# Kernel tuning notes

Measured on AMD Instinct MI355X. Metric: run time of the kernel, lower is better.

## Reference

```python
import jax, jax.numpy as jnp
import numpy as np

HIDDEN = 2048
HEADS = 16
HEAD_DIM = HIDDEN // HEADS  # 128
B, S = 2, 2048
SCALE = 1.0 / np.sqrt(HEAD_DIM)


def setup_inputs() -> dict:
    key = jax.random.key(0)
    ks = jax.random.split(key, 9)
    x = jax.random.normal(ks[0], (B, S, HIDDEN), dtype=jnp.float32)
    # causal mask, broadcastable to [B, 1(group), H, S, S]
    mask = jnp.tril(jnp.ones((S, S), dtype=bool))[None, None, None, :, :]
    mask = jnp.broadcast_to(mask, (B, 1, 1, S, S))
    s = 0.02
    Wq = jax.random.normal(ks[1], (HIDDEN, HIDDEN), dtype=jnp.float32) * s
    bq = jnp.zeros((HIDDEN,), dtype=jnp.float32)
    Wk = jax.random.normal(ks[2], (HIDDEN, HEAD_DIM), dtype=jnp.float32) * s
    bk = jnp.zeros((HEAD_DIM,), dtype=jnp.float32)
    Wv = jax.random.normal(ks[3], (HIDDEN, HEAD_DIM), dtype=jnp.float32) * s
    bv = jnp.zeros((HEAD_DIM,), dtype=jnp.float32)
    Wo = jax.random.normal(ks[4], (HIDDEN, HIDDEN), dtype=jnp.float32) * s
    bo = jnp.zeros((HIDDEN,), dtype=jnp.float32)
    return {"x": x, "mask": mask, "Wq": Wq, "bq": bq, "Wk": Wk, "bk": bk,
            "Wv": Wv, "bv": bv, "Wo": Wo, "bo": bo}


def reference(x, mask, Wq, bq, Wk, bk, Wv, bv, Wo, bo):
    b, s, _ = x.shape
    q = (x @ Wq + bq).reshape(b, s, HEADS, HEAD_DIM)   # [b,s,h,d]
    k = x @ Wk + bk                                    # [b,t,d] single shared KV head
    v = x @ Wv + bv                                    # [b,t,d]
    # scores: [b, h, s, t]; add group dim to match mask [b,1,h,s,t]
    scores = jnp.einsum('bshd,btd->bhst', q, k) * SCALE
    scores = scores[:, None]                            # [b,1,h,s,t]
    scores = jnp.where(mask, scores, jnp.float32(-jnp.inf))
    att = jax.nn.softmax(scores, axis=-1)[:, 0]         # [b,h,s,t] (dropout eval = identity)
    out = jnp.einsum('bhst,btd->bshd', att, v).reshape(b, s, HIDDEN)
    return out @ Wo + bo
```

## Files before the change

kernel.cpp:

```cpp
#include <hip/hip_runtime.h>


#define HIDDEN 2048
#define NHEADS 16
#define HDIM 128
#define BATCH 2
#define SEQ 2048
#define SCALE_L2E 0.1275258653864023f

typedef __attribute__((ext_vector_type(8))) short bfrag;
typedef __attribute__((ext_vector_type(4))) float facc;

__device__ __forceinline__ unsigned short f2bf(float f) {
  unsigned int u = __float_as_uint(f);
  u += 0x7fffu + ((u >> 16) & 1u);
  return (unsigned short)(u >> 16);
}

__device__ __forceinline__ unsigned int cvt_pk_bf16(float lo, float hi) {
  unsigned int r;
  asm("v_cvt_pk_bf16_f32 %0, %1, %2" : "=v"(r) : "v"(lo), "v"(hi));
  return r;
}

__device__ __forceinline__ void gl_lds16(const void* g, void* l) {
  __builtin_amdgcn_global_load_lds(
      (const __attribute__((address_space(1))) void*)g,
      (__attribute__((address_space(3))) void*)l, 16, 0, 0);
}

__global__ __launch_bounds__(256) void cvt_bf16(const float* __restrict__ in,
                                                unsigned int* __restrict__ out, int n4) {
  int i = blockIdx.x * 256 + threadIdx.x;
  if (i >= n4) return;
  float4 v = ((const float4*)in)[i];
  uint2 o = {cvt_pk_bf16(v.x, v.y), cvt_pk_bf16(v.z, v.w)};
  ((uint2*)out)[i] = o;
}

__global__ __launch_bounds__(256) void transpose_cvt2(const float* __restrict__ W0,
                                                      short* __restrict__ T0,
                                                      const float* __restrict__ W1,
                                                      short* __restrict__ T1,
                                                      int K, int N) {
  const float* W = blockIdx.z ? W1 : W0;
  short* WT = blockIdx.z ? T1 : T0;
  __shared__ float t[32][33];
  int tx = threadIdx.x & 31, ty = threadIdx.x >> 5;
  int n0 = blockIdx.x * 32, k0 = blockIdx.y * 32;
#pragma unroll
  for (int j = 0; j < 4; ++j)
    t[ty + j * 8][tx] = W[(size_t)(k0 + ty + j * 8) * N + n0 + tx];
  __syncthreads();
#pragma unroll
  for (int j = 0; j < 4; ++j)
    WT[(size_t)(n0 + ty + j * 8) * K + k0 + tx] = (short)f2bf(t[tx][ty + j * 8]);
}

#define GEMM_STAGE(buf, kt, A, BT, Kdim)                                       \
  _Pragma("unroll") for (int it = 0; it < 4; ++it) {                           \
    int bc = (w * 4 + it) * 64;                                                \
    int C = bc + l;                                                            \
    int row = C >> 3, c = C & 7;                                               \
    int gofs = (kt) * 64 + ((c ^ (row & 7)) << 3);                             \
    gl_lds16((A) + (size_t)(m0 + row) * (Kdim) + gofs, &Al[buf][bc * 8]);      \
    gl_lds16((BT) + (size_t)(n0 + row) * (Kdim) + gofs, &Bl[buf][bc * 8]);     \
  }

#define GEMM_PIPE_LOOP(A, BT, Kdim)                                            \
  facc acc[4][4] = {};                                                         \
  const int nkt = (Kdim) >> 6;                                                 \
  GEMM_STAGE(0, 0, A, BT, Kdim)                                                \
  __syncthreads();                                                             \
  for (int kt = 0; kt < nkt; ++kt) {                                           \
    const int cur = kt & 1;                                                    \
    if (kt + 1 < nkt) { GEMM_STAGE(cur ^ 1, kt + 1, A, BT, Kdim) }             \
    __builtin_amdgcn_s_setprio(1);                                             \
    _Pragma("unroll") for (int ks = 0; ks < 2; ++ks) {                         \
      bfrag af[4], bf[4];                                                      \
      _Pragma("unroll") for (int mt = 0; mt < 4; ++mt) {                       \
        int row = wr * 64 + mt * 16 + l15;                                     \
        int c = ks * 4 + l4;                                                   \
        af[mt] = *(const bfrag*)&Al[cur][row * 64 + ((c ^ (row & 7)) << 3)];   \
      }                                                                        \
      _Pragma("unroll") for (int nt = 0; nt < 4; ++nt) {                       \
        int row = wc * 64 + nt * 16 + l15;                                     \
        int c = ks * 4 + l4;                                                   \
        bf[nt] = *(const bfrag*)&Bl[cur][row * 64 + ((c ^ (row & 7)) << 3)];   \
      }                                                                        \
      _Pragma("unroll") for (int mt = 0; mt < 4; ++mt)                         \
          _Pragma("unroll") for (int nt = 0; nt < 4; ++nt)                     \
              acc[mt][nt] = __builtin_amdgcn_mfma_f32_16x16x32_bf16(           \
                  af[mt], bf[nt], acc[mt][nt], 0, 0, 0);                       \
    }                                                                          \
    __builtin_amdgcn_s_setprio(0);                                             \
    __syncthreads();                                                           \
  }

__global__ __launch_bounds__(256) void gemm_qkv(const short* __restrict__ A,
                                                const short* __restrict__ BT,
                                                const float* __restrict__ bq,
                                                const float* __restrict__ bk,
                                                const float* __restrict__ bv,
                                                unsigned short* __restrict__ Qb,
                                                unsigned short* __restrict__ Kb,
                                                unsigned short* __restrict__ Vtb,
                                                int M, int K) {
  __shared__ __align__(16) short Al[2][128 * 64];
  __shared__ __align__(16) short Bl[2][128 * 64];
  const int tid = threadIdx.x;
  const int w = tid >> 6, l = tid & 63;
  const int wr = w >> 1, wc = w & 1;
  const int l15 = l & 15, l4 = l >> 4;
  const int m0 = blockIdx.x * 128, n0 = blockIdx.y * 128;
  GEMM_PIPE_LOOP(A, BT, K)
#pragma unroll
  for (int mt = 0; mt < 4; ++mt) {
#pragma unroll
    for (int nt = 0; nt < 4; ++nt) {
#pragma unroll
      for (int r = 0; r < 4; ++r) {
        int row = m0 + wr * 64 + mt * 16 + l4 * 4 + r;
        int col = n0 + wc * 64 + nt * 16 + l15;
        if (col < HIDDEN) {
          Qb[(size_t)row * HIDDEN + col] = f2bf(acc[mt][nt][r] + bq[col]);
        } else if (col < HIDDEN + HDIM) {
          int lc = col - HIDDEN;
          Kb[(size_t)row * HDIM + lc] = f2bf(acc[mt][nt][r] + bk[lc]);
        } else {
          int lc = col - HIDDEN - HDIM;
          Vtb[(size_t)lc * M + row] = f2bf(acc[mt][nt][r] + bv[lc]);
        }
      }
    }
  }
}

__global__ __launch_bounds__(256) void gemm_out(const short* __restrict__ A,
                                                const short* __restrict__ BT,
                                                const float* __restrict__ bias,
                                                float* __restrict__ Cout,
                                                int M, int N, int K) {
  __shared__ __align__(16) short Al[2][128 * 64];
  __shared__ __align__(16) short Bl[2][128 * 64];
  const int tid = threadIdx.x;
  const int w = tid >> 6, l = tid & 63;
  const int wr = w >> 1, wc = w & 1;
  const int l15 = l & 15, l4 = l >> 4;
  const int m0 = blockIdx.x * 128, n0 = blockIdx.y * 128;
  GEMM_PIPE_LOOP(A, BT, K)
#pragma unroll
  for (int mt = 0; mt < 4; ++mt)
#pragma unroll
    for (int nt = 0; nt < 4; ++nt)
#pragma unroll
      for (int r = 0; r < 4; ++r) {
        int row = m0 + wr * 64 + mt * 16 + l4 * 4 + r;
        int col = n0 + wc * 64 + nt * 16 + l15;
        Cout[(size_t)row * N + col] = acc[mt][nt][r] + bias[col];
      }
}

__global__ __launch_bounds__(256, 2) void attn_kernel(const short* __restrict__ Q,
                                                      const short* __restrict__ Kg,
                                                      const short* __restrict__ Vt,
                                                      unsigned short* __restrict__ O) {
  __shared__ __align__(16) short Kl[2][64 * 128];
  __shared__ __align__(16) short Vl[2][128 * 64];
  __shared__ __align__(16) char Pl[4][2048];
  const int tid = threadIdx.x;
  const int w = tid >> 6, l = tid & 63;
  const int l15 = l & 15, l4 = l >> 4;
  const int h = blockIdx.y, b = blockIdx.z;

#define STAGE_KV(buf, t)                                                            \
  do {                                                                              \
    const int kv0_ = (t) << 6;                                                      \
    _Pragma("unroll") for (int it = 0; it < 4; ++it) {                              \
      int bc = (w * 4 + it) * 64;                                                   \
      int C = bc + l;                                                               \
      int key = C >> 4, c = C & 15;                                                 \
      gl_lds16(Kg + (size_t)(b * SEQ + kv0_ + key) * HDIM + ((c ^ (key & 7)) << 3), \
               &Kl[buf][bc * 8]);                                                   \
    }                                                                               \
    _Pragma("unroll") for (int it = 0; it < 4; ++it) {                              \
      int bc = (w * 4 + it) * 64;                                                   \
      int C = bc + l;                                                               \
      int d = C >> 3, c = C & 7;                                                    \
      gl_lds16(Vt + (size_t)d * (BATCH * SEQ) + b * SEQ + kv0_ + ((c ^ (d & 7)) << 3), \
               &Vl[buf][bc * 8]);                                                   \
    }                                                                               \
  } while (0)

  for (int pass = 0; pass < 2; ++pass) {
    const int qtile = (pass == 0) ? (int)blockIdx.x : 31 - (int)blockIdx.x;
    const int q0 = qtile * 64;
    const int qw = q0 + w * 16;

    bfrag aq[4];
#pragma unroll
    for (int kk = 0; kk < 4; ++kk)
      aq[kk] = *(const bfrag*)(Q + (size_t)(b * SEQ + qw + l15) * HIDDEN +
                               h * HDIM + kk * 32 + l4 * 8);

    facc accO[8] = {};
    float mrow = -INFINITY, lrow = 0.f;
    const int nkv = qtile + 1;

    STAGE_KV(0, 0);
    __syncthreads();

    for (int t = 0; t < nkv; ++t) {
      const int cur = t & 1;
      if (t + 1 < nkv) STAGE_KV(cur ^ 1, t + 1);
      const int kv0 = t << 6;

      facc sac[4] = {};
      __builtin_amdgcn_s_setprio(1);
#pragma unroll
      for (int kk = 0; kk < 4; ++kk) {
        int c = kk * 4 + l4;
#pragma unroll
        for (int kt = 0; kt < 4; ++kt) {
          int key = kt * 16 + l15;
          bfrag ak = *(const bfrag*)&Kl[cur][key * 128 + ((c ^ (key & 7)) << 3)];
          sac[kt] = __builtin_amdgcn_mfma_f32_16x16x32_bf16(ak, aq[kk], sac[kt], 0, 0, 0);
        }
      }
      __builtin_amdgcn_s_setprio(0);

      const int qg = qw + l15;
      const bool needmask = (kv0 + 63 > qw);
      float p[4][4];
      float mt = -INFINITY;
#pragma unroll
      for (int kt = 0; kt < 4; ++kt)
#pragma unroll
        for (int r = 0; r < 4; ++r) {
          float v = sac[kt][r] * SCALE_L2E;
          if (needmask) {
            int keyg = kv0 + kt * 16 + l4 * 4 + r;
            v = (keyg <= qg) ? v : -INFINITY;
          }
          p[kt][r] = v;
          mt = fmaxf(mt, v);
        }
      mt = fmaxf(mt, __shfl_xor(mt, 16));
      mt = fmaxf(mt, __shfl_xor(mt, 32));
      float mn = fmaxf(mrow, mt);
      float f = exp2f(mrow - mn);
      mrow = mn;
      float ps = 0.f;
#pragma unroll
      for (int kt = 0; kt < 4; ++kt)
#pragma unroll
        for (int r = 0; r < 4; ++r) {
          p[kt][r] = exp2f(p[kt][r] - mn);
          ps += p[kt][r];
        }
      ps += __shfl_xor(ps, 16);
      ps += __shfl_xor(ps, 32);
      lrow = lrow * f + ps;
      float fr[4];
#pragma unroll
      for (int r = 0; r < 4; ++r) fr[r] = __shfl(f, l4 * 4 + r);

      char* pw = &Pl[w][0];
#pragma unroll
      for (int kt = 0; kt < 4; ++kt)
#pragma unroll
        for (int rp = 0; rp < 2; ++rp) {
          unsigned int u = cvt_pk_bf16(p[kt][2 * rp], p[kt][2 * rp + 1]);
          int byte = (l15 * 128 + (kt * 16 + l4 * 4 + 2 * rp) * 2) ^ ((l15 & 7) << 4);
          *(unsigned int*)(pw + byte) = u;
        }
#pragma unroll
      for (int nt = 0; nt < 8; ++nt)
#pragma unroll
        for (int r = 0; r < 4; ++r) accO[nt][r] *= fr[r];

      __builtin_amdgcn_s_setprio(1);
#pragma unroll
      for (int kc = 0; kc < 2; ++kc) {
        bfrag pa = *(const bfrag*)(&Pl[w][0] +
                                   ((l15 * 128 + (kc * 32 + l4 * 8) * 2) ^ ((l15 & 7) << 4)));
#pragma unroll
        for (int nt = 0; nt < 8; ++nt) {
          int d = nt * 16 + l15;
          int cslot = (kc * 4 + l4) ^ (d & 7);
          bfrag bv = *(const bfrag*)&Vl[cur][d * 64 + (cslot << 3)];
          accO[nt] = __builtin_amdgcn_mfma_f32_16x16x32_bf16(pa, bv, accO[nt], 0, 0, 0);
        }
      }
      __builtin_amdgcn_s_setprio(0);
      __syncthreads();
    }

    float inv = 1.f / lrow;
#pragma unroll
    for (int r = 0; r < 4; ++r) {
      float invr = __shfl(inv, l4 * 4 + r);
      int row = qw + l4 * 4 + r;
#pragma unroll
      for (int nt = 0; nt < 8; ++nt)
        O[(size_t)(b * SEQ + row) * HIDDEN + h * HDIM + nt * 16 + l15] =
            f2bf(accO[nt][r] * invr);
    }
  }
#undef STAGE_KV
}

extern "C" void kernel_launch(void* const* d_in, const int* in_sizes, int n_in,
                              void* d_out, int out_size, void* d_ws, size_t ws_size,
                              hipStream_t stream) {
  const float* x = (const float*)d_in[0];
  const float* Wq = (const float*)d_in[2];
  const float* bq = (const float*)d_in[3];
  const float* Wk = (const float*)d_in[4];
  const float* bk = (const float*)d_in[5];
  const float* Wv = (const float*)d_in[6];
  const float* bv = (const float*)d_in[7];
  const float* Wo = (const float*)d_in[8];
  const float* bo = (const float*)d_in[9];
  float* out = (float*)d_out;

  const size_t MS = (size_t)BATCH * SEQ;
  char* ws = (char*)d_ws;
  short* xb = (short*)ws;      ws += MS * HIDDEN * 2;
  short* WqkvT = (short*)ws;   ws += (size_t)(HIDDEN + 2 * HDIM) * HIDDEN * 2;
  short* WoT = (short*)ws;     ws += (size_t)HIDDEN * HIDDEN * 2;
  short* Qb = (short*)ws;      ws += MS * HIDDEN * 2;
  short* Kb = (short*)ws;      ws += MS * HDIM * 2;
  short* Vtb = (short*)ws;     ws += (size_t)HDIM * MS * 2;
  short* Ab = (short*)ws;      ws += MS * HIDDEN * 2;

  cvt_bf16<<<(int)(MS * HIDDEN / 4 / 256), 256, 0, stream>>>(
      x, (unsigned int*)xb, (int)(MS * HIDDEN / 4));
  transpose_cvt2<<<dim3(HIDDEN / 32, HIDDEN / 32, 2), 256, 0, stream>>>(
      Wq, WqkvT, Wo, WoT, HIDDEN, HIDDEN);
  transpose_cvt2<<<dim3(HDIM / 32, HIDDEN / 32, 2), 256, 0, stream>>>(
      Wk, WqkvT + (size_t)HIDDEN * HIDDEN, Wv, WqkvT + (size_t)(HIDDEN + HDIM) * HIDDEN,
      HIDDEN, HDIM);

  gemm_qkv<<<dim3(32, 18), 256, 0, stream>>>(xb, WqkvT, bq, bk, bv,
                                             (unsigned short*)Qb, (unsigned short*)Kb,
                                             (unsigned short*)Vtb, (int)MS, HIDDEN);

  attn_kernel<<<dim3(16, NHEADS, BATCH), 256, 0, stream>>>(Qb, Kb, Vtb,
                                                           (unsigned short*)Ab);

  gemm_out<<<dim3(32, 16), 256, 0, stream>>>(Ab, WoT, bo, out, (int)MS, HIDDEN, HIDDEN);
}
```

Before: 223.2 us.

## Replace GEMMs with 256x256-tile, 8-wave, 4-slot pipelined kernels

Both the QKV projection and output projection GEMMs move from 128x128 tiles with 4 waves and a two-buffer K=64 pipeline to 256x256 tiles with 8 waves, K=32 stages and a four-slot LDS ring. Loads are staged three steps ahead with explicit vmcnt/lgkmcnt waits and barriers interleaved between MFMA half-blocks. The goal is more operand reuse per LDS byte and more latency hiding. The trade-off is that grids shrink to 144 and 128 blocks on a 256-CU part, leaving many CUs idle, with one block per CU due to the large LDS use.

Measured after the change: 249.8 us. 11.9% more time.

```diff
diff --git a/kernel.cpp b/kernel.cpp
--- a/kernel.cpp
+++ b/kernel.cpp
@@ -57,108 +57,147 @@
     WT[(size_t)(n0 + ty + j * 8) * K + k0 + tx] = (short)f2bf(t[tx][ty + j * 8]);
 }
 
-#define GEMM_STAGE(buf, kt, A, BT, Kdim)                                       \
-  _Pragma("unroll") for (int it = 0; it < 4; ++it) {                           \
-    int bc = (w * 4 + it) * 64;                                                \
-    int C = bc + l;                                                            \
-    int row = C >> 3, c = C & 7;                                               \
-    int gofs = (kt) * 64 + ((c ^ (row & 7)) << 3);                             \
-    gl_lds16((A) + (size_t)(m0 + row) * (Kdim) + gofs, &Al[buf][bc * 8]);      \
-    gl_lds16((BT) + (size_t)(n0 + row) * (Kdim) + gofs, &Bl[buf][bc * 8]);     \
-  }
-
-#define GEMM_PIPE_LOOP(A, BT, Kdim)                                            \
-  facc acc[4][4] = {};                                                         \
-  const int nkt = (Kdim) >> 6;                                                 \
-  GEMM_STAGE(0, 0, A, BT, Kdim)                                                \
-  __syncthreads();                                                             \
-  for (int kt = 0; kt < nkt; ++kt) {                                           \
-    const int cur = kt & 1;                                                    \
-    if (kt + 1 < nkt) { GEMM_STAGE(cur ^ 1, kt + 1, A, BT, Kdim) }             \
-    __builtin_amdgcn_s_setprio(1);                                             \
-    _Pragma("unroll") for (int ks = 0; ks < 2; ++ks) {                         \
-      bfrag af[4], bf[4];                                                      \
-      _Pragma("unroll") for (int mt = 0; mt < 4; ++mt) {                       \
-        int row = wr * 64 + mt * 16 + l15;                                     \
-        int c = ks * 4 + l4;                                                   \
-        af[mt] = *(const bfrag*)&Al[cur][row * 64 + ((c ^ (row & 7)) << 3)];   \
-      }                                                                        \
-      _Pragma("unroll") for (int nt = 0; nt < 4; ++nt) {                       \
-        int row = wc * 64 + nt * 16 + l15;                                     \
-        int c = ks * 4 + l4;                                                   \
-        bf[nt] = *(const bfrag*)&Bl[cur][row * 64 + ((c ^ (row & 7)) << 3)];   \
-      }                                                                        \
-      _Pragma("unroll") for (int mt = 0; mt < 4; ++mt)                         \
-          _Pragma("unroll") for (int nt = 0; nt < 4; ++nt)                     \
-              acc[mt][nt] = __builtin_amdgcn_mfma_f32_16x16x32_bf16(           \
-                  af[mt], bf[nt], acc[mt][nt], 0, 0, 0);                       \
-    }                                                                          \
-    __builtin_amdgcn_s_setprio(0);                                             \
-    __syncthreads();                                                           \
-  }
-
-__global__ __launch_bounds__(256) void gemm_qkv(const short* __restrict__ A,
-                                                const short* __restrict__ BT,
-                                                const float* __restrict__ bq,
-                                                const float* __restrict__ bk,
-                                                const float* __restrict__ bv,
-                                                unsigned short* __restrict__ Qb,
-                                                unsigned short* __restrict__ Kb,
-                                                unsigned short* __restrict__ Vtb,
-                                                int M, int K) {
-  __shared__ __align__(16) short Al[2][128 * 64];
-  __shared__ __align__(16) short Bl[2][128 * 64];
+
+#define SBAR() __builtin_amdgcn_s_barrier()
+#define LGKM0()                                        \
+  do {                                                 \
+    asm volatile("s_waitcnt lgkmcnt(0)" ::: "memory"); \
+    __builtin_amdgcn_sched_barrier(0);                 \
+  } while (0)
+#define WAIT_VM(n) asm volatile("s_waitcnt vmcnt(" #n ")" ::: "memory")
+
+#define STG_A(s)                                                            \
+  _Pragma("unroll") for (int it_ = 0; it_ < 2; ++it_) {                     \
+    int rb_ = w * 32 + it_ * 16;                                            \
+    gl_lds16(Ag + (size_t)(m0 + rb_ + (l >> 2)) * Kdim + (s) * 32 +         \
+                 (((l & 3) ^ ((l >> 3) & 3)) << 3),                         \
+             &As[(s) & 3][rb_ * 32]);                                       \
+  }
+#define STG_B(s)                                                            \
+  _Pragma("unroll") for (int it_ = 0; it_ < 2; ++it_) {                     \
+    int rb_ = w * 32 + it_ * 16;                                            \
+    gl_lds16(Bg + (size_t)(n0 + rb_ + (l >> 2)) * Kdim + (s) * 32 +         \
+                 (((l & 3) ^ ((l >> 3) & 3)) << 3),                         \
+             &Bs[(s) & 3][rb_ * 32]);                                       \
+  }
+#define RD_A(slot_, qm_)                                                    \
+  _Pragma("unroll") for (int mt = 0; mt < 4; ++mt) {                        \
+    int r_ = wm * 128 + (qm_) * 64 + mt * 16 + l15;                         \
+    af[mt] = *(const bfrag*)&As[slot_][r_ * 32 + ((l4 ^ ((r_ >> 1) & 3)) << 3)]; \
+  }
+#define RD_B(slot_)                                                         \
+  _Pragma("unroll") for (int nt = 0; nt < 4; ++nt) {                        \
+    int r_ = wn * 64 + nt * 16 + l15;                                       \
+    bf[nt] = *(const bfrag*)&Bs[slot_][r_ * 32 + ((l4 ^ ((r_ >> 1) & 3)) << 3)]; \
+  }
+#define MFMA16(qm_)                                                         \
+  __builtin_amdgcn_s_setprio(1);                                            \
+  _Pragma("unroll") for (int mt = 0; mt < 4; ++mt)                          \
+      _Pragma("unroll") for (int nt = 0; nt < 4; ++nt)                      \
+          acc[qm_][mt][nt] = __builtin_amdgcn_mfma_f32_16x16x32_bf16(       \
+              af[mt], bf[nt], acc[qm_][mt][nt], 0, 0, 0);                   \
+  __builtin_amdgcn_s_setprio(0);
+
+#define GEMM256_MAIN(Ag, Bg, Kdim)                                          \
+  facc acc[2][4][4] = {};                                                   \
+  const int NS = (Kdim) >> 5;                                               \
+  const int NT = NS >> 1;                                                   \
+  STG_A(0); STG_B(0); STG_A(1); STG_B(1); STG_A(2); STG_B(2);               \
+  WAIT_VM(8);                                                               \
+  SBAR();                                                                   \
+  for (int t = 0; t < NT; ++t) {                                            \
+    const int sl0 = (2 * t) & 3, sl1 = (2 * t + 1) & 3;                     \
+    bfrag af[4], bf[4];                                                     \
+                                                \
+    RD_A(sl0, 0); RD_B(sl0);                                                \
+    if (2 * t + 3 < NS) { STG_A(2 * t + 3); }                               \
+    SBAR(); LGKM0(); MFMA16(0);                                             \
+    SBAR();                                                                 \
+                                     \
+    RD_A(sl0, 1);                                                           \
+    if (2 * t + 3 < NS) { STG_B(2 * t + 3); }                               \
+    SBAR(); LGKM0(); MFMA16(1);                                             \
+    if (t < NT - 1) { WAIT_VM(8); } else { WAIT_VM(0); }                    \
+    SBAR();                                                                 \
+                                              \
+    RD_A(sl1, 0); RD_B(sl1);                                                \
+    if (2 * t + 4 < NS) { STG_A(2 * t + 4); }                               \
+    SBAR(); LGKM0(); MFMA16(0);                                             \
+    SBAR();                                                                 \
+                                              \
+    RD_A(sl1, 1);                                                           \
+    if (2 * t + 4 < NS) { STG_B(2 * t + 4); }                               \
+    SBAR(); LGKM0(); MFMA16(1);                                             \
+    if (t < NT - 2) { WAIT_VM(8); }                                         \
+    else if (t == NT - 2) { WAIT_VM(4); }                                   \
+    SBAR();                                                                 \
+  }
+
+__global__ __launch_bounds__(512, 1) void gemm_qkv256(const short* __restrict__ Ag,
+                                                      const short* __restrict__ Bg,
+                                                      const float* __restrict__ bq,
+                                                      const float* __restrict__ bk,
+                                                      const float* __restrict__ bv,
+                                                      unsigned short* __restrict__ Qb,
+                                                      unsigned short* __restrict__ Kb,
+                                                      unsigned short* __restrict__ Vtb,
+                                                      int M, int Kdim) {
+  __shared__ __align__(16) short As[4][256 * 32];
+  __shared__ __align__(16) short Bs[4][256 * 32];
   const int tid = threadIdx.x;
   const int w = tid >> 6, l = tid & 63;
-  const int wr = w >> 1, wc = w & 1;
+  const int wm = w >> 2, wn = w & 3;
   const int l15 = l & 15, l4 = l >> 4;
-  const int m0 = blockIdx.x * 128, n0 = blockIdx.y * 128;
-  GEMM_PIPE_LOOP(A, BT, K)
-#pragma unroll
-  for (int mt = 0; mt < 4; ++mt) {
-#pragma unroll
-    for (int nt = 0; nt < 4; ++nt) {
-#pragma unroll
-      for (int r = 0; r < 4; ++r) {
-        int row = m0 + wr * 64 + mt * 16 + l4 * 4 + r;
-        int col = n0 + wc * 64 + nt * 16 + l15;
-        if (col < HIDDEN) {
-          Qb[(size_t)row * HIDDEN + col] = f2bf(acc[mt][nt][r] + bq[col]);
-        } else if (col < HIDDEN + HDIM) {
-          int lc = col - HIDDEN;
-          Kb[(size_t)row * HDIM + lc] = f2bf(acc[mt][nt][r] + bk[lc]);
-        } else {
-          int lc = col - HIDDEN - HDIM;
-          Vtb[(size_t)lc * M + row] = f2bf(acc[mt][nt][r] + bv[lc]);
-        }
-      }
-    }
-  }
-}
-
-__global__ __launch_bounds__(256) void gemm_out(const short* __restrict__ A,
-                                                const short* __restrict__ BT,
-                                                const float* __restrict__ bias,
-                                                float* __restrict__ Cout,
-                                                int M, int N, int K) {
-  __shared__ __align__(16) short Al[2][128 * 64];
-  __shared__ __align__(16) short Bl[2][128 * 64];
+  const int m0 = blockIdx.x * 256, n0 = blockIdx.y * 256;
+  GEMM256_MAIN(Ag, Bg, Kdim)
+#pragma unroll
+  for (int qm = 0; qm < 2; ++qm)
+#pragma unroll
+    for (int mt = 0; mt < 4; ++mt)
+#pragma unroll
+      for (int nt = 0; nt < 4; ++nt)
+#pragma unroll
+        for (int r = 0; r < 4; ++r) {
+          int row = m0 + wm * 128 + qm * 64 + mt * 16 + l4 * 4 + r;
+          int col = n0 + wn * 64 + nt * 16 + l15;
+          float v = acc[qm][mt][nt][r];
+          if (col < HIDDEN) {
+            Qb[(size_t)row * HIDDEN + col] = f2bf(v + bq[col]);
+          } else if (col < HIDDEN + HDIM) {
+            int lc = col - HIDDEN;
+            Kb[(size_t)row * HDIM + lc] = f2bf(v + bk[lc]);
+          } else {
+            int lc = col - HIDDEN - HDIM;
+            Vtb[(size_t)lc * M + row] = f2bf(v + bv[lc]);
+          }
+        }
+}
+
+__global__ __launch_bounds__(512, 1) void gemm_out256(const short* __restrict__ Ag,
+                                                      const short* __restrict__ Bg,
+                                                      const float* __restrict__ bias,
+                                                      float* __restrict__ Cout,
+                                                      int M, int N, int Kdim) {
+  __shared__ __align__(16) short As[4][256 * 32];
+  __shared__ __align__(16) short Bs[4][256 * 32];
   const int tid = threadIdx.x;
   const int w = tid >> 6, l = tid & 63;
-  const int wr = w >> 1, wc = w & 1;
+  const int wm = w >> 2, wn = w & 3;
   const int l15 = l & 15, l4 = l >> 4;
-  const int m0 = blockIdx.x * 128, n0 = blockIdx.y * 128;
-  GEMM_PIPE_LOOP(A, BT, K)
-#pragma unroll
-  for (int mt = 0; mt < 4; ++mt)
-#pragma unroll
-    for (int nt = 0; nt < 4; ++nt)
-#pragma unroll
-      for (int r = 0; r < 4; ++r) {
-        int row = m0 + wr * 64 + mt * 16 + l4 * 4 + r;
-        int col = n0 + wc * 64 + nt * 16 + l15;
-        Cout[(size_t)row * N + col] = acc[mt][nt][r] + bias[col];
-      }
+  const int m0 = blockIdx.x * 256, n0 = blockIdx.y * 256;
+  GEMM256_MAIN(Ag, Bg, Kdim)
+#pragma unroll
+  for (int qm = 0; qm < 2; ++qm)
+#pragma unroll
+    for (int mt = 0; mt < 4; ++mt)
+#pragma unroll
+      for (int nt = 0; nt < 4; ++nt)
+#pragma unroll
+        for (int r = 0; r < 4; ++r) {
+          int row = m0 + wm * 128 + qm * 64 + mt * 16 + l4 * 4 + r;
+          int col = n0 + wn * 64 + nt * 16 + l15;
+          Cout[(size_t)row * N + col] = acc[qm][mt][nt][r] + bias[col];
+        }
 }
 
 __global__ __launch_bounds__(256, 2) void attn_kernel(const short* __restrict__ Q,
@@ -342,12 +381,12 @@
       Wk, WqkvT + (size_t)HIDDEN * HIDDEN, Wv, WqkvT + (size_t)(HIDDEN + HDIM) * HIDDEN,
       HIDDEN, HDIM);
 
-  gemm_qkv<<<dim3(32, 18), 256, 0, stream>>>(xb, WqkvT, bq, bk, bv,
-                                             (unsigned short*)Qb, (unsigned short*)Kb,
-                                             (unsigned short*)Vtb, (int)MS, HIDDEN);
+  gemm_qkv256<<<dim3(16, 9), 512, 0, stream>>>(xb, WqkvT, bq, bk, bv,
+                                               (unsigned short*)Qb, (unsigned short*)Kb,
+                                               (unsigned short*)Vtb, (int)MS, HIDDEN);
 
   attn_kernel<<<dim3(16, NHEADS, BATCH), 256, 0, stream>>>(Qb, Kb, Vtb,
                                                            (unsigned short*)Ab);
 
-  gemm_out<<<dim3(32, 16), 256, 0, stream>>>(Ab, WoT, bo, out, (int)MS, HIDDEN, HIDDEN);
-}
+  gemm_out256<<<dim3(16, 8), 512, 0, stream>>>(Ab, WoT, bo, out, (int)MS, HIDDEN, HIDDEN);
+}
```
